# Kernel optimization log

Hardware: AMD Instinct MI355X
Metric: run time of the kernel (lower is better)

Reference implementation:

```python
import jax, jax.numpy as jnp
import numpy as np

N, E, D = 50000, 1000000, 64
EPS = 1e-5


def setup_inputs() -> dict:
    key = jax.random.key(0)
    ks = jax.random.split(key, 20)
    inp = {
        "x": jax.random.normal(ks[0], (N, D), dtype=jnp.float32),
        "e": jax.random.uniform(ks[1], (E,), dtype=jnp.float32),
        "edge_index": jax.random.randint(ks[2], (2, E), 0, N, dtype=jnp.int64),
    }
    dims = [(3 * D, D), (D, D), (D, D), (D, D)]
    for i, (fi, fo) in enumerate(dims):
        s = 1.0 / np.sqrt(fi)
        inp[f"W{i+1}"] = jax.random.uniform(ks[3 + 4 * i], (fi, fo), minval=-s, maxval=s, dtype=jnp.float32)
        inp[f"b{i+1}"] = jax.random.uniform(ks[4 + 4 * i], (fo,), minval=-s, maxval=s, dtype=jnp.float32)
        inp[f"g{i+1}"] = jnp.ones((fo,), dtype=jnp.float32)
        inp[f"bt{i+1}"] = jnp.zeros((fo,), dtype=jnp.float32)
    return inp


def _layer(h, W, b, g, bt):
    h = h @ W + b
    mu = jnp.mean(h, axis=-1, keepdims=True)
    var = jnp.mean(jnp.square(h - mu), axis=-1, keepdims=True)
    h = (h - mu) * jax.lax.rsqrt(var + EPS) * g + bt
    return jax.nn.relu(h)


def reference(x, e, edge_index, W1, b1, g1, bt1, W2, b2, g2, bt2, W3, b3, g3, bt3, W4, b4, g4, bt4):
    start, end = edge_index[0], edge_index[1]
    we = e[:, None]  # [E,1]
    # aggregate weighted neighbor features on each side
    mi = jax.ops.segment_sum(we * x[start], end, num_segments=x.shape[0])
    mo = jax.ops.segment_sum(we * x[end], start, num_segments=x.shape[0])
    h = jnp.concatenate([mi, mo, x], axis=1)  # [N, 3D]
    h = _layer(h, W1, b1, g1, bt1)
    h = _layer(h, W2, b2, g2, bt2)
    h = _layer(h, W3, b3, g3, bt3)
    h = _layer(h, W4, b4, g4, bt4)
    return h
```

## Files before the change

kernel.cpp:

```cpp
#include <hip/hip_runtime.h>

#define DD 64
#define EPSV 1e-5f

__device__ __forceinline__ float rlane_f(float v, int k) {
    return __int_as_float(__builtin_amdgcn_readlane(__float_as_int(v), k));
}

__global__ void detect_idx_kernel(const void* __restrict__ idx, int* __restrict__ flag,
                                  int nsample, int n_nodes) {
    const long long* p = (const long long*)idx;
    int bad = 0;
    for (int i = threadIdx.x; i < nsample; i += blockDim.x) {
        long long v = p[i];
        if (v < 0 || v >= (long long)n_nodes) bad = 1;
    }
    __shared__ int sbad;
    if (threadIdx.x == 0) sbad = 0;
    __syncthreads();
    if (bad) atomicOr(&sbad, 1);
    __syncthreads();
    if (threadIdx.x == 0) *flag = sbad ? 0 : 1;
}

__global__ __launch_bounds__(256) void hist_kernel(
    const void* __restrict__ idx, const int* __restrict__ flag,
    int* __restrict__ cnt0, int* __restrict__ cnt1, int n_edges) {
    const bool is64 = (*flag != 0);
    const long long* p64 = (const long long*)idx;
    const int*       p32 = (const int*)idx;
    int tid = blockIdx.x * blockDim.x + threadIdx.x;
    int stride = gridDim.x * blockDim.x;
    for (int ed = tid; ed < n_edges; ed += stride) {
        int s, t;
        if (is64) { s = (int)p64[ed]; t = (int)p64[n_edges + ed]; }
        else      { s = p32[ed];      t = p32[n_edges + ed]; }
        atomicAdd(&cnt0[t], 1);
        atomicAdd(&cnt1[s], 1);
    }
}

#define SC 52
__global__ __launch_bounds__(1024) void scan_kernel(
    const int* __restrict__ cnt0, const int* __restrict__ cnt1,
    int* __restrict__ offs0, int* __restrict__ offs1,
    int* __restrict__ cur0, int* __restrict__ cur1, int n) {
    const int* cnt = blockIdx.x ? cnt1 : cnt0;
    int* offs = blockIdx.x ? offs1 : offs0;
    int* cur  = blockIdx.x ? cur1  : cur0;
    const int t = threadIdx.x;
    const int base = t * SC;
    int m = n - base; if (m > SC) m = SC; if (m < 0) m = 0;

    int v[SC];
    int sum = 0;
    if (m == SC) {
        const int4* c4 = (const int4*)(cnt + base);
        #pragma unroll
        for (int i = 0; i < SC / 4; ++i) {
            int4 q = c4[i];
            v[4*i] = q.x; v[4*i+1] = q.y; v[4*i+2] = q.z; v[4*i+3] = q.w;
        }
        #pragma unroll
        for (int i = 0; i < SC; ++i) sum += v[i];
    } else {
        for (int i = 0; i < m; ++i) sum += cnt[base + i];
    }

    const int lane = t & 63, wid = t >> 6;
    int s = sum;
    #pragma unroll
    for (int d = 1; d < 64; d <<= 1) { int u = __shfl_up(s, d, 64); if (lane >= d) s += u; }

    __shared__ int wtot[16];
    if (lane == 63) wtot[wid] = s;
    __syncthreads();
    if (t < 16) {
        int w = wtot[t];
        int sw = w;
        #pragma unroll
        for (int d = 1; d < 16; d <<= 1) { int u = __shfl_up(sw, d, 64); if (t >= d) sw += u; }
        wtot[t] = sw - w;
    }
    __syncthreads();

    int run = wtot[wid] + (s - sum);
    if (m == SC) {
        int4* o4 = (int4*)(offs + base);
        int4* c4w = (int4*)(cur + base);
        #pragma unroll
        for (int i = 0; i < SC / 4; ++i) {
            int4 q;
            q.x = run; run += v[4*i];
            q.y = run; run += v[4*i+1];
            q.z = run; run += v[4*i+2];
            q.w = run; run += v[4*i+3];
            o4[i] = q; c4w[i] = q;
        }
        if (base + SC == n) offs[n] = run;
    } else if (m > 0) {
        for (int i = 0; i < m; ++i) {
            int c = cnt[base + i];
            offs[base + i] = run;
            cur[base + i]  = run;
            run += c;
        }
        if (base + m == n) offs[n] = run;
    }
}

__global__ __launch_bounds__(256) void fill_kernel(
    const void* __restrict__ idx, const float* __restrict__ e, const int* __restrict__ flag,
    int* __restrict__ cur0, int* __restrict__ cur1,
    int2* __restrict__ pay0, int2* __restrict__ pay1, int n_edges) {
    const bool is64 = (*flag != 0);
    const long long* p64 = (const long long*)idx;
    const int*       p32 = (const int*)idx;
    int tid = blockIdx.x * blockDim.x + threadIdx.x;
    int stride = gridDim.x * blockDim.x;
    for (int ed = tid; ed < n_edges; ed += stride) {
        int s, t;
        if (is64) { s = (int)p64[ed]; t = (int)p64[n_edges + ed]; }
        else      { s = p32[ed];      t = p32[n_edges + ed]; }
        int wbits = __float_as_int(e[ed]);
        int p0 = atomicAdd(&cur0[t], 1);
        pay0[p0] = make_int2(s, wbits);
        int p1 = atomicAdd(&cur1[s], 1);
        pay1[p1] = make_int2(t, wbits);
    }
}

__global__ __launch_bounds__(256) void gather_kernel(
    const float* __restrict__ x,
    const int2* __restrict__ pay0, const int2* __restrict__ pay1,
    const int* __restrict__ offs0, const int* __restrict__ offs1,
    float* __restrict__ mi, float* __restrict__ mo, int n) {
    const int wid = threadIdx.x >> 6, lane = threadIdx.x & 63;
    const int gid = blockIdx.x * 4 + wid;
    if (gid >= 2 * n) return;
    const int dir = gid & 1, node = gid >> 1;
    const int* offs = dir ? offs1 : offs0;
    const int2* pay = dir ? pay1 : pay0;
    float* dst = dir ? mo : mi;

    const int o0 = offs[node], o1 = offs[node + 1];
    float acc = 0.0f;
    for (int b = o0; b < o1; b += 64) {
        int2 pl = make_int2(0, 0);
        if (b + lane < o1) pl = pay[b + lane];
        const int cnt = min(64, o1 - b);
        #pragma unroll 4
        for (int j = 0; j < cnt; ++j) {
            int src  = __builtin_amdgcn_readlane(pl.x, j);
            float w  = __int_as_float(__builtin_amdgcn_readlane(pl.y, j));
            acc = fmaf(w, x[src * DD + lane], acc);
        }
    }
    dst[node * DD + lane] = acc;
}

__global__ __launch_bounds__(256) void scatter_kernel(
    const float* __restrict__ x, const float* __restrict__ e,
    const void* __restrict__ idx, const int* __restrict__ flag,
    float* __restrict__ mi, float* __restrict__ mo, int n_edges) {
    const int lane  = threadIdx.x & 63;
    const int slot  = (blockIdx.x * blockDim.x + threadIdx.x) >> 6;
    const int nslot = (gridDim.x * blockDim.x) >> 6;
    const bool is64 = (*flag != 0);
    const long long* p64 = (const long long*)idx;
    const int*       p32 = (const int*)idx;
    for (int ed = slot; ed < n_edges; ed += nslot) {
        int s, t;
        if (is64) { s = (int)p64[ed]; t = (int)p64[n_edges + ed]; }
        else      { s = p32[ed];      t = p32[n_edges + ed]; }
        float w  = e[ed];
        unsafeAtomicAdd(&mi[t * DD + lane], w * x[s * DD + lane]);
        unsafeAtomicAdd(&mo[s * DD + lane], w * x[t * DD + lane]);
    }
}

#define NPW 13
#define MWAVES 16
#define WT1_STRIDE 196
#define WT_STRIDE  68

template<int N>
__device__ __forceinline__ void accum64(const float4* __restrict__ wp,
                                        const float (&h)[N], float (&acc)[N]) {
    #pragma unroll 2
    for (int kb = 0; kb < 16; ++kb) {
        float4 w4 = wp[kb];
        int k0 = kb << 2;
        #pragma unroll
        for (int m = 0; m < N; ++m) acc[m] = fmaf(w4.x, rlane_f(h[m], k0), acc[m]);
        #pragma unroll
        for (int m = 0; m < N; ++m) acc[m] = fmaf(w4.y, rlane_f(h[m], k0 + 1), acc[m]);
        #pragma unroll
        for (int m = 0; m < N; ++m) acc[m] = fmaf(w4.z, rlane_f(h[m], k0 + 2), acc[m]);
        #pragma unroll
        for (int m = 0; m < N; ++m) acc[m] = fmaf(w4.w, rlane_f(h[m], k0 + 3), acc[m]);
    }
}

__device__ __forceinline__ float ln_relu(float v, float g, float bt) {
    float s = v;
    #pragma unroll
    for (int off = 32; off; off >>= 1) s += __shfl_xor(s, off, 64);
    float mu = s * (1.0f / 64.0f);
    float d = v - mu;
    float s2 = d * d;
    #pragma unroll
    for (int off = 32; off; off >>= 1) s2 += __shfl_xor(s2, off, 64);
    float r = d * rsqrtf(s2 * (1.0f / 64.0f) + EPSV) * g + bt;
    return fmaxf(r, 0.0f);
}

__global__ __launch_bounds__(1024) void fused_mlp2(
    const float* __restrict__ mi, const float* __restrict__ mo, const float* __restrict__ x,
    const float* __restrict__ W1, const float* __restrict__ b1, const float* __restrict__ g1, const float* __restrict__ bt1,
    const float* __restrict__ W2, const float* __restrict__ b2, const float* __restrict__ g2, const float* __restrict__ bt2,
    const float* __restrict__ W3, const float* __restrict__ b3, const float* __restrict__ g3, const float* __restrict__ bt3,
    const float* __restrict__ W4, const float* __restrict__ b4, const float* __restrict__ g4, const float* __restrict__ bt4,
    float* __restrict__ out, int n_nodes) {

    __shared__ float sWT1[64 * WT1_STRIDE];
    __shared__ float sWT2[64 * WT_STRIDE];
    __shared__ float sWT3[64 * WT_STRIDE];
    __shared__ float sWT4[64 * WT_STRIDE];
    __shared__ float sB[4][3][64];

    const int tid = threadIdx.x;
    for (int i = tid; i < 192 * 64; i += 1024) {
        int k = i >> 6, j = i & 63;
        sWT1[j * WT1_STRIDE + k] = W1[i];
    }
    for (int i = tid; i < 64 * 64; i += 1024) {
        int k = i >> 6, j = i & 63;
        sWT2[j * WT_STRIDE + k] = W2[i];
        sWT3[j * WT_STRIDE + k] = W3[i];
        sWT4[j * WT_STRIDE + k] = W4[i];
    }
    if (tid < 64) {
        int j = tid;
        sB[0][0][j] = b1[j]; sB[0][1][j] = g1[j]; sB[0][2][j] = bt1[j];
        sB[1][0][j] = b2[j]; sB[1][1][j] = g2[j]; sB[1][2][j] = bt2[j];
        sB[2][0][j] = b3[j]; sB[2][1][j] = g3[j]; sB[2][2][j] = bt3[j];
        sB[3][0][j] = b4[j]; sB[3][1][j] = g4[j]; sB[3][2][j] = bt4[j];
    }
    __syncthreads();

    const int wid = tid >> 6, lane = tid & 63;
    const int gw = blockIdx.x * MWAVES + wid;
    const int nw = gridDim.x * MWAVES;
    const float4* wt1 = (const float4*)&sWT1[lane * WT1_STRIDE];
    const float4* wt2 = (const float4*)&sWT2[lane * WT_STRIDE];
    const float4* wt3 = (const float4*)&sWT3[lane * WT_STRIDE];
    const float4* wt4 = (const float4*)&sWT4[lane * WT_STRIDE];

    const int ngroups = (n_nodes + NPW - 1) / NPW;
    for (int grp = gw; grp < ngroups; grp += nw) {
        const int n0 = grp * NPW;

        float hmi[NPW], hmo[NPW], hx[NPW];
        #pragma unroll
        for (int m = 0; m < NPW; ++m) {
            int n = n0 + m; if (n >= n_nodes) n = n_nodes - 1;
            hmi[m] = mi[n * DD + lane];
            hmo[m] = mo[n * DD + lane];
            hx[m]  = x[n * DD + lane];
        }

        float acc[NPW], h[NPW];

        {
            float bj = sB[0][0][lane];
            #pragma unroll
            for (int m = 0; m < NPW; ++m) acc[m] = bj;
            accum64(wt1 +  0, hmi, acc);
            accum64(wt1 + 16, hmo, acc);
            accum64(wt1 + 32, hx,  acc);
            float gj = sB[0][1][lane], btj = sB[0][2][lane];
            #pragma unroll
            for (int m = 0; m < NPW; ++m) h[m] = ln_relu(acc[m], gj, btj);
        }

        const float4* wts[3] = { wt2, wt3, wt4 };
        #pragma unroll
        for (int l = 0; l < 3; ++l) {
            float bj = sB[l + 1][0][lane];
            #pragma unroll
            for (int m = 0; m < NPW; ++m) acc[m] = bj;
            accum64(wts[l], h, acc);
            float gj = sB[l + 1][1][lane], btj = sB[l + 1][2][lane];
            #pragma unroll
            for (int m = 0; m < NPW; ++m) h[m] = ln_relu(acc[m], gj, btj);
        }

        #pragma unroll
        for (int m = 0; m < NPW; ++m) {
            int n = n0 + m;
            if (n < n_nodes) out[n * DD + lane] = h[m];
        }
    }
}

extern "C" void kernel_launch(void* const* d_in, const int* in_sizes, int n_in,
                              void* d_out, int out_size, void* d_ws, size_t ws_size,
                              hipStream_t stream) {
    const float* x   = (const float*)d_in[0];
    const float* e   = (const float*)d_in[1];
    const void*  idx = d_in[2];
    const float* W1 = (const float*)d_in[3],  *b1 = (const float*)d_in[4],
               * g1 = (const float*)d_in[5],  *bt1 = (const float*)d_in[6];
    const float* W2 = (const float*)d_in[7],  *b2 = (const float*)d_in[8],
               * g2 = (const float*)d_in[9],  *bt2 = (const float*)d_in[10];
    const float* W3 = (const float*)d_in[11], *b3 = (const float*)d_in[12],
               * g3 = (const float*)d_in[13], *bt3 = (const float*)d_in[14];
    const float* W4 = (const float*)d_in[15], *b4 = (const float*)d_in[16],
               * g4 = (const float*)d_in[17], *bt4 = (const float*)d_in[18];
    float* out = (float*)d_out;

    const int n_nodes = in_sizes[0] / DD;
    const int n_edges = in_sizes[1];

    float* mi = (float*)d_ws;
    float* mo = mi + (size_t)n_nodes * DD;
    int*  flag = (int*)(mo + (size_t)n_nodes * DD);
    char* p = (char*)(flag + 4);
    const int offs_pad = (n_nodes + 1 + 3) & ~3;
    int2* pay0 = (int2*)p;            p += (size_t)n_edges * sizeof(int2);
    int2* pay1 = (int2*)p;            p += (size_t)n_edges * sizeof(int2);
    int* cnt0  = (int*)p;             p += (size_t)n_nodes * 4;
    int* cnt1  = (int*)p;             p += (size_t)n_nodes * 4;
    int* offs0 = (int*)p;             p += (size_t)offs_pad * 4;
    int* offs1 = (int*)p;             p += (size_t)offs_pad * 4;
    int* cur0  = (int*)p;             p += (size_t)n_nodes * 4;
    int* cur1  = (int*)p;             p += (size_t)n_nodes * 4;
    const size_t need = (size_t)(p - (char*)d_ws);

    detect_idx_kernel<<<1, 256, 0, stream>>>(idx, flag, 4096, n_nodes);

    if (ws_size >= need) {
        hipMemsetAsync(cnt0, 0, (size_t)2 * n_nodes * 4, stream);
        hist_kernel<<<2048, 256, 0, stream>>>(idx, flag, cnt0, cnt1, n_edges);
        scan_kernel<<<2, 1024, 0, stream>>>(cnt0, cnt1, offs0, offs1, cur0, cur1, n_nodes);
        fill_kernel<<<2048, 256, 0, stream>>>(idx, e, flag, cur0, cur1, pay0, pay1, n_edges);
        const int nblocks = (2 * n_nodes + 3) / 4;
        gather_kernel<<<nblocks, 256, 0, stream>>>(x, pay0, pay1, offs0, offs1, mi, mo, n_nodes);
    } else {
        hipMemsetAsync(d_ws, 0, (size_t)2 * n_nodes * DD * sizeof(float), stream);
        scatter_kernel<<<4096, 256, 0, stream>>>(x, e, idx, flag, mi, mo, n_edges);
    }

    fused_mlp2<<<256, 1024, 0, stream>>>(
        mi, mo, x,
        W1, b1, g1, bt1, W2, b2, g2, bt2, W3, b3, g3, bt3, W4, b4, g4, bt4,
        out, n_nodes);
}
```

Baseline: 601.3 us.

## Read MLP weights directly from global memory and launch one node group per wave

The fused MLP kernel no longer stages transposed weight matrices in shared memory. Each lane now reads its weight column straight from global memory with coalesced row accesses, relying on L1/L2 caching. The grid also changes from a persistent 256x1024 launch to one wave per 13-node group with 512-thread blocks. This removes the per-block shared-memory fill, the barrier and the LDS footprint, which should raise occupancy. In exchange every k step issues a scalar global load instead of a float4 LDS read, adding load latency and cache pressure.

```diff
diff --git a/kernel.cpp b/kernel.cpp
--- a/kernel.cpp
+++ b/kernel.cpp
@@ -180,25 +180,15 @@
 }
 
 #define NPW 13
-#define MWAVES 16
-#define WT1_STRIDE 196
-#define WT_STRIDE  68
 
 template<int N>
-__device__ __forceinline__ void accum64(const float4* __restrict__ wp,
-                                        const float (&h)[N], float (&acc)[N]) {
-    #pragma unroll 2
-    for (int kb = 0; kb < 16; ++kb) {
-        float4 w4 = wp[kb];
-        int k0 = kb << 2;
-        #pragma unroll
-        for (int m = 0; m < N; ++m) acc[m] = fmaf(w4.x, rlane_f(h[m], k0), acc[m]);
-        #pragma unroll
-        for (int m = 0; m < N; ++m) acc[m] = fmaf(w4.y, rlane_f(h[m], k0 + 1), acc[m]);
-        #pragma unroll
-        for (int m = 0; m < N; ++m) acc[m] = fmaf(w4.z, rlane_f(h[m], k0 + 2), acc[m]);
-        #pragma unroll
-        for (int m = 0; m < N; ++m) acc[m] = fmaf(w4.w, rlane_f(h[m], k0 + 3), acc[m]);
+__device__ __forceinline__ void accumG(const float* __restrict__ wcol,
+                                       const float (&h)[N], float (&acc)[N]) {
+    #pragma unroll 8
+    for (int k = 0; k < 64; ++k) {
+        float w = wcol[k * 64];
+        #pragma unroll
+        for (int m = 0; m < N; ++m) acc[m] = fmaf(w, rlane_f(h[m], k), acc[m]);
     }
 }
 
@@ -215,7 +205,7 @@
     return fmaxf(r, 0.0f);
 }
 
-__global__ __launch_bounds__(1024) void fused_mlp2(
+__global__ __launch_bounds__(512) void fused_mlp4(
     const float* __restrict__ mi, const float* __restrict__ mo, const float* __restrict__ x,
     const float* __restrict__ W1, const float* __restrict__ b1, const float* __restrict__ g1, const float* __restrict__ bt1,
     const float* __restrict__ W2, const float* __restrict__ b2, const float* __restrict__ g2, const float* __restrict__ bt2,
@@ -223,84 +213,67 @@
     const float* __restrict__ W4, const float* __restrict__ b4, const float* __restrict__ g4, const float* __restrict__ bt4,
     float* __restrict__ out, int n_nodes) {
 
-    __shared__ float sWT1[64 * WT1_STRIDE];
-    __shared__ float sWT2[64 * WT_STRIDE];
-    __shared__ float sWT3[64 * WT_STRIDE];
-    __shared__ float sWT4[64 * WT_STRIDE];
-    __shared__ float sB[4][3][64];
-
-    const int tid = threadIdx.x;
-    for (int i = tid; i < 192 * 64; i += 1024) {
-        int k = i >> 6, j = i & 63;
-        sWT1[j * WT1_STRIDE + k] = W1[i];
-    }
-    for (int i = tid; i < 64 * 64; i += 1024) {
-        int k = i >> 6, j = i & 63;
-        sWT2[j * WT_STRIDE + k] = W2[i];
-        sWT3[j * WT_STRIDE + k] = W3[i];
-        sWT4[j * WT_STRIDE + k] = W4[i];
-    }
-    if (tid < 64) {
-        int j = tid;
-        sB[0][0][j] = b1[j]; sB[0][1][j] = g1[j]; sB[0][2][j] = bt1[j];
-        sB[1][0][j] = b2[j]; sB[1][1][j] = g2[j]; sB[1][2][j] = bt2[j];
-        sB[2][0][j] = b3[j]; sB[2][1][j] = g3[j]; sB[2][2][j] = bt3[j];
-        sB[3][0][j] = b4[j]; sB[3][1][j] = g4[j]; sB[3][2][j] = bt4[j];
-    }
-    __syncthreads();
-
-    const int wid = tid >> 6, lane = tid & 63;
-    const int gw = blockIdx.x * MWAVES + wid;
-    const int nw = gridDim.x * MWAVES;
-    const float4* wt1 = (const float4*)&sWT1[lane * WT1_STRIDE];
-    const float4* wt2 = (const float4*)&sWT2[lane * WT_STRIDE];
-    const float4* wt3 = (const float4*)&sWT3[lane * WT_STRIDE];
-    const float4* wt4 = (const float4*)&sWT4[lane * WT_STRIDE];
-
+    const int wid = threadIdx.x >> 6, lane = threadIdx.x & 63;
+    const int gw = blockIdx.x * 8 + wid;
     const int ngroups = (n_nodes + NPW - 1) / NPW;
-    for (int grp = gw; grp < ngroups; grp += nw) {
-        const int n0 = grp * NPW;
-
-        float hmi[NPW], hmo[NPW], hx[NPW];
-        #pragma unroll
-        for (int m = 0; m < NPW; ++m) {
-            int n = n0 + m; if (n >= n_nodes) n = n_nodes - 1;
-            hmi[m] = mi[n * DD + lane];
-            hmo[m] = mo[n * DD + lane];
-            hx[m]  = x[n * DD + lane];
-        }
-
-        float acc[NPW], h[NPW];
-
-        {
-            float bj = sB[0][0][lane];
-            #pragma unroll
-            for (int m = 0; m < NPW; ++m) acc[m] = bj;
-            accum64(wt1 +  0, hmi, acc);
-            accum64(wt1 + 16, hmo, acc);
-            accum64(wt1 + 32, hx,  acc);
-            float gj = sB[0][1][lane], btj = sB[0][2][lane];
-            #pragma unroll
-            for (int m = 0; m < NPW; ++m) h[m] = ln_relu(acc[m], gj, btj);
-        }
-
-        const float4* wts[3] = { wt2, wt3, wt4 };
-        #pragma unroll
-        for (int l = 0; l < 3; ++l) {
-            float bj = sB[l + 1][0][lane];
-            #pragma unroll
-            for (int m = 0; m < NPW; ++m) acc[m] = bj;
-            accum64(wts[l], h, acc);
-            float gj = sB[l + 1][1][lane], btj = sB[l + 1][2][lane];
-            #pragma unroll
-            for (int m = 0; m < NPW; ++m) h[m] = ln_relu(acc[m], gj, btj);
-        }
-
-        #pragma unroll
-        for (int m = 0; m < NPW; ++m) {
-            int n = n0 + m;
-            if (n < n_nodes) out[n * DD + lane] = h[m];
-        }
+    if (gw >= ngroups) return;
+    const int n0 = gw * NPW;
+
+    float hmi[NPW], hmo[NPW], hx[NPW];
+    #pragma unroll
+    for (int m = 0; m < NPW; ++m) {
+        int n = n0 + m; if (n >= n_nodes) n = n_nodes - 1;
+        hmi[m] = mi[n * DD + lane];
+        hmo[m] = mo[n * DD + lane];
+        hx[m]  = x[n * DD + lane];
+    }
+
+    float acc[NPW], h[NPW];
+
+    {
+        float bj = b1[lane];
+        #pragma unroll
+        for (int m = 0; m < NPW; ++m) acc[m] = bj;
+        accumG(W1 + lane,             hmi, acc);
+        accumG(W1 + 64 * DD + lane,   hmo, acc);
+        accumG(W1 + 128 * DD + lane,  hx,  acc);
+        float gj = g1[lane], btj = bt1[lane];
+        #pragma unroll
+        for (int m = 0; m < NPW; ++m) h[m] = ln_relu(acc[m], gj, btj);
+    }
+
+    {
+        float bj = b2[lane];
+        #pragma unroll
+        for (int m = 0; m < NPW; ++m) acc[m] = bj;
+        accumG(W2 + lane, h, acc);
+        float gj = g2[lane], btj = bt2[lane];
+        #pragma unroll
+        for (int m = 0; m < NPW; ++m) h[m] = ln_relu(acc[m], gj, btj);
+    }
+    {
+        float bj = b3[lane];
+        #pragma unroll
+        for (int m = 0; m < NPW; ++m) acc[m] = bj;
+        accumG(W3 + lane, h, acc);
+        float gj = g3[lane], btj = bt3[lane];
+        #pragma unroll
+        for (int m = 0; m < NPW; ++m) h[m] = ln_relu(acc[m], gj, btj);
+    }
+    {
+        float bj = b4[lane];
+        #pragma unroll
+        for (int m = 0; m < NPW; ++m) acc[m] = bj;
+        accumG(W4 + lane, h, acc);
+        float gj = g4[lane], btj = bt4[lane];
+        #pragma unroll
+        for (int m = 0; m < NPW; ++m) h[m] = ln_relu(acc[m], gj, btj);
+    }
+
+    #pragma unroll
+    for (int m = 0; m < NPW; ++m) {
+        int n = n0 + m;
+        if (n < n_nodes) out[n * DD + lane] = h[m];
     }
 }
 
@@ -352,7 +325,9 @@
         scatter_kernel<<<4096, 256, 0, stream>>>(x, e, idx, flag, mi, mo, n_edges);
     }
 
-    fused_mlp2<<<256, 1024, 0, stream>>>(
+    const int ngroups = (n_nodes + NPW - 1) / NPW;
+    const int mblocks = (ngroups + 7) / 8;
+    fused_mlp4<<<mblocks, 512, 0, stream>>>(
         mi, mo, x,
         W1, b1, g1, bt1, W2, b2, g2, bt2, W3, b3, g3, bt3, W4, b4, g4, bt4,
         out, n_nodes);
```

New measurement: 604.3 us. Within noise of the previous version (+0.5%).
